# Kernel optimization log

Hardware: AMD Instinct MI355X
Metric: run time of the kernel (lower is better)

Reference implementation:

```python
import jax, jax.numpy as jnp
import numpy as np
from math import log

X_SIZE, Y_SIZE, W_SIZE = 512, 512, 256
SIGMA = 2.0
TIME_CONST = 1000.0 / log(SIGMA)  # default time_constant = 1000/log(sigma)


def setup_inputs() -> dict:
    key = jax.random.key(0)
    k1, k2 = jax.random.split(key)
    x = jax.random.normal(k1, (W_SIZE,), dtype=jnp.float32)
    W = jax.random.normal(k2, (X_SIZE, Y_SIZE, W_SIZE), dtype=jnp.float32)
    return {"x": x, "W": W, "time_step": 100}


def reference(x, W, time_step):
    # per-cell L2 distance: (X_SIZE, Y_SIZE)
    d = jnp.linalg.norm(x - W, ord=2, axis=-1)
    flat = jnp.argmin(d)
    wx, wy = jnp.unravel_index(flat, (X_SIZE, Y_SIZE))
    # torch.meshgrid default 'ij' indexing
    GX, GY = jnp.meshgrid(
        jnp.arange(X_SIZE, dtype=jnp.float32),
        jnp.arange(Y_SIZE, dtype=jnp.float32),
        indexing="ij",
    )
    decay = SIGMA * jnp.exp(-jnp.float32(time_step) / TIME_CONST)
    denom = 2.0 * decay * decay
    # Faithful to torch: GX.T[wx, wy] == wy and GY.T[wx, wy] == wx
    distx = (GX - wy.astype(jnp.float32)) ** 2
    disty = (GY - wx.astype(jnp.float32)) ** 2
    h = (jnp.exp(-distx / denom) * jnp.exp(-disty / denom)).T
    return h, (wx, wy)
```

## Files before the change

kernel.cpp:

```cpp
#include <hip/hip_runtime.h>
#include <math.h>

#define XS 512
#define YS 512
#define WDIM 256
#define NCELLS (XS * YS)
#define K1_BLOCKS 2048
#define K1_THREADS 256
#define NTHREADS (K1_BLOCKS * K1_THREADS)
#define NWAVES (NTHREADS / 64)
#define K1_ITERS 32
#define NSLOTS 32
#define SLOT_STRIDE 16

typedef float vfloat4 __attribute__((ext_vector_type(4)));

__global__ __launch_bounds__(K1_THREADS) void som_dist_kernel(
    const float* __restrict__ x,
    const float* __restrict__ W,
    unsigned long long* __restrict__ ws) {
  const int tid = threadIdx.x;
  const int lane = tid & 63;
  const int waveInBlock = tid >> 6;
  const int gtid = blockIdx.x * K1_THREADS + tid;
  const int w = gtid >> 6;

  const vfloat4 xv = ((const vfloat4*)x)[lane];
  const vfloat4* __restrict__ W4 = (const vfloat4*)W;

  float acc[K1_ITERS];
#pragma unroll
  for (int it = 0; it < K1_ITERS; ++it) {
    const vfloat4 v = W4[(size_t)gtid + (size_t)it * NTHREADS];
    const float dx = xv.x - v.x;
    const float dy = xv.y - v.y;
    const float dz = xv.z - v.z;
    const float dw = xv.w - v.w;
    acc[it] = dx * dx + dy * dy + dz * dz + dw * dw;
  }

  const bool b0 = (lane & 1) != 0;
  const bool b1 = (lane & 2) != 0;
  const bool b2 = (lane & 4) != 0;
  const bool b3 = (lane & 8) != 0;
  const bool b4 = (lane & 16) != 0;

#pragma unroll
  for (int j = 0; j < 16; ++j) {
    const float keep = b0 ? acc[2 * j + 1] : acc[2 * j];
    const float send = b0 ? acc[2 * j] : acc[2 * j + 1];
    acc[j] = keep + __shfl_xor(send, 1, 64);
  }
#pragma unroll
  for (int j = 0; j < 8; ++j) {
    const float keep = b1 ? acc[2 * j + 1] : acc[2 * j];
    const float send = b1 ? acc[2 * j] : acc[2 * j + 1];
    acc[j] = keep + __shfl_xor(send, 2, 64);
  }
#pragma unroll
  for (int j = 0; j < 4; ++j) {
    const float keep = b2 ? acc[2 * j + 1] : acc[2 * j];
    const float send = b2 ? acc[2 * j] : acc[2 * j + 1];
    acc[j] = keep + __shfl_xor(send, 4, 64);
  }
#pragma unroll
  for (int j = 0; j < 2; ++j) {
    const float keep = b3 ? acc[2 * j + 1] : acc[2 * j];
    const float send = b3 ? acc[2 * j] : acc[2 * j + 1];
    acc[j] = keep + __shfl_xor(send, 8, 64);
  }
  {
    const float keep = b4 ? acc[1] : acc[0];
    const float send = b4 ? acc[0] : acc[1];
    acc[0] = keep + __shfl_xor(send, 16, 64);
  }
  const float v = acc[0] + __shfl_xor(acc[0], 32, 64);

  const int cell = w + (lane & 31) * NWAVES;

  unsigned long long packed =
      ((unsigned long long)__float_as_uint(v) << 32) | (unsigned int)cell;

#pragma unroll
  for (int off = 32; off > 0; off >>= 1) {
    const unsigned long long o = __shfl_xor(packed, off, 64);
    packed = (o < packed) ? o : packed;
  }

  __shared__ unsigned long long sbest[K1_THREADS / 64];
  if (lane == 0) sbest[waveInBlock] = packed;
  __syncthreads();
  if (tid == 0) {
    unsigned long long m = sbest[0];
#pragma unroll
    for (int i = 1; i < K1_THREADS / 64; ++i) {
      const unsigned long long v2 = sbest[i];
      m = (v2 < m) ? v2 : m;
    }
    atomicMin(ws + (blockIdx.x & (NSLOTS - 1)) * SLOT_STRIDE, m);
  }
}

__global__ __launch_bounds__(256) void som_h_kernel(
    const unsigned long long* __restrict__ ws,
    const int* __restrict__ time_step,
    float* __restrict__ out) {
  const int t = threadIdx.x;
  const int lane = t & 63;

  unsigned long long v = ws[(lane & (NSLOTS - 1)) * SLOT_STRIDE];
#pragma unroll
  for (int off = 1; off < 32; off <<= 1) {
    const unsigned long long o = __shfl_xor(v, off, 64);
    v = (o < v) ? o : v;
  }

  const int flat = (int)(v & 0xFFFFFFFFULL);
  const int wx = flat >> 9;
  const int wy = flat & (YS - 1);

  const float ts = (float)(*time_step);
  const float TIME_CONST = 1442.6950408889634f;
  const float decay = 2.0f * expf(-ts / TIME_CONST);
  const float denom = 2.0f * decay * decay;
  const float inv = -1.0f / denom;

  const int e = blockIdx.x * 1024 + t * 4;
  const int i = e >> 9;
  const int j0 = e & (YS - 1);
  const float di = (float)(i - wx);
  const float di2 = di * di;

  const float d0 = (float)(j0 + 0 - wy);
  const float d1 = (float)(j0 + 1 - wy);
  const float d2 = (float)(j0 + 2 - wy);
  const float d3 = (float)(j0 + 3 - wy);
  vfloat4 r;
  r.x = expf((di2 + d0 * d0) * inv);
  r.y = expf((di2 + d1 * d1) * inv);
  r.z = expf((di2 + d2 * d2) * inv);
  r.w = expf((di2 + d3 * d3) * inv);
  ((vfloat4*)out)[e >> 2] = r;

  if (blockIdx.x == 0 && t == 0) {
    out[NCELLS] = (float)wx;
    out[NCELLS + 1] = (float)wy;
  }
}

extern "C" void kernel_launch(void* const* d_in, const int* in_sizes, int n_in,
                              void* d_out, int out_size, void* d_ws, size_t ws_size,
                              hipStream_t stream) {
  const float* x = (const float*)d_in[0];
  const float* W = (const float*)d_in[1];
  const int* ts = (const int*)d_in[2];
  float* out = (float*)d_out;
  unsigned long long* ws = (unsigned long long*)d_ws;

  (void)hipMemsetAsync(ws, 0xFF, NSLOTS * SLOT_STRIDE * 8, stream);
  som_dist_kernel<<<K1_BLOCKS, K1_THREADS, 0, stream>>>(x, W, ws);
  som_h_kernel<<<NCELLS / 1024, 256, 0, stream>>>(ws, ts, out);
}
```

Before: 375.0 us.

## Process W rows in chunks of eight with nontemporal loads and running min

The distance kernel now loads W in four chunks of eight vectors instead of all 32 at once. Each chunk is reduced with a shorter transpose-style shuffle tree and then folded into a per-lane running minimum. Loads switch to nontemporal hints to avoid polluting cache on the single-use 256MB stream. The change lowers register pressure but also reduces the number of loads in flight per thread, which could hurt latency hiding on this bandwidth-bound kernel. It also adds more shuffles per element.

Result: faster. 349.8 us (-6.7%).

```diff
diff --git a/kernel.cpp b/kernel.cpp
--- a/kernel.cpp
+++ b/kernel.cpp
@@ -9,7 +9,8 @@
 #define K1_THREADS 256
 #define NTHREADS (K1_BLOCKS * K1_THREADS)
 #define NWAVES (NTHREADS / 64)
-#define K1_ITERS 32
+#define NCHUNKS 4
+#define CPER 8
 #define NSLOTS 32
 #define SLOT_STRIDE 16
 
@@ -28,58 +29,55 @@
   const vfloat4 xv = ((const vfloat4*)x)[lane];
   const vfloat4* __restrict__ W4 = (const vfloat4*)W;
 
-  float acc[K1_ITERS];
-#pragma unroll
-  for (int it = 0; it < K1_ITERS; ++it) {
-    const vfloat4 v = W4[(size_t)gtid + (size_t)it * NTHREADS];
-    const float dx = xv.x - v.x;
-    const float dy = xv.y - v.y;
-    const float dz = xv.z - v.z;
-    const float dw = xv.w - v.w;
-    acc[it] = dx * dx + dy * dy + dz * dz + dw * dw;
-  }
+  float bestD = 3.4e38f;
+  int bestI = 0;
 
   const bool b0 = (lane & 1) != 0;
   const bool b1 = (lane & 2) != 0;
   const bool b2 = (lane & 4) != 0;
-  const bool b3 = (lane & 8) != 0;
-  const bool b4 = (lane & 16) != 0;
+  const int r7 = lane & 7;
 
 #pragma unroll
-  for (int j = 0; j < 16; ++j) {
-    const float keep = b0 ? acc[2 * j + 1] : acc[2 * j];
-    const float send = b0 ? acc[2 * j] : acc[2 * j + 1];
-    acc[j] = keep + __shfl_xor(send, 1, 64);
+  for (int c = 0; c < NCHUNKS; ++c) {
+    float acc[CPER];
+#pragma unroll
+    for (int j = 0; j < CPER; ++j) {
+      const vfloat4 v = __builtin_nontemporal_load(
+          W4 + (size_t)gtid + (size_t)(c * CPER + j) * NTHREADS);
+      const float dx = xv.x - v.x;
+      const float dy = xv.y - v.y;
+      const float dz = xv.z - v.z;
+      const float dw = xv.w - v.w;
+      acc[j] = dx * dx + dy * dy + dz * dz + dw * dw;
+    }
+
+#pragma unroll
+    for (int j = 0; j < 4; ++j) {
+      const float keep = b0 ? acc[2 * j + 1] : acc[2 * j];
+      const float send = b0 ? acc[2 * j] : acc[2 * j + 1];
+      acc[j] = keep + __shfl_xor(send, 1, 64);
+    }
+#pragma unroll
+    for (int j = 0; j < 2; ++j) {
+      const float keep = b1 ? acc[2 * j + 1] : acc[2 * j];
+      const float send = b1 ? acc[2 * j] : acc[2 * j + 1];
+      acc[j] = keep + __shfl_xor(send, 2, 64);
+    }
+    {
+      const float keep = b2 ? acc[1] : acc[0];
+      const float send = b2 ? acc[0] : acc[1];
+      acc[0] = keep + __shfl_xor(send, 4, 64);
+    }
+    float v = acc[0];
+    v += __shfl_xor(v, 8, 64);
+    v += __shfl_xor(v, 16, 64);
+    v += __shfl_xor(v, 32, 64);
+
+    if (v < bestD) { bestD = v; bestI = w + (c * CPER + r7) * NWAVES; }
   }
-#pragma unroll
-  for (int j = 0; j < 8; ++j) {
-    const float keep = b1 ? acc[2 * j + 1] : acc[2 * j];
-    const float send = b1 ? acc[2 * j] : acc[2 * j + 1];
-    acc[j] = keep + __shfl_xor(send, 2, 64);
-  }
-#pragma unroll
-  for (int j = 0; j < 4; ++j) {
-    const float keep = b2 ? acc[2 * j + 1] : acc[2 * j];
-    const float send = b2 ? acc[2 * j] : acc[2 * j + 1];
-    acc[j] = keep + __shfl_xor(send, 4, 64);
-  }
-#pragma unroll
-  for (int j = 0; j < 2; ++j) {
-    const float keep = b3 ? acc[2 * j + 1] : acc[2 * j];
-    const float send = b3 ? acc[2 * j] : acc[2 * j + 1];
-    acc[j] = keep + __shfl_xor(send, 8, 64);
-  }
-  {
-    const float keep = b4 ? acc[1] : acc[0];
-    const float send = b4 ? acc[0] : acc[1];
-    acc[0] = keep + __shfl_xor(send, 16, 64);
-  }
-  const float v = acc[0] + __shfl_xor(acc[0], 32, 64);
-
-  const int cell = w + (lane & 31) * NWAVES;
 
   unsigned long long packed =
-      ((unsigned long long)__float_as_uint(v) << 32) | (unsigned int)cell;
+      ((unsigned long long)__float_as_uint(bestD) << 32) | (unsigned int)bestI;
 
 #pragma unroll
   for (int off = 32; off > 0; off >>= 1) {
```
